# Kernel optimization log

Hardware: AMD Instinct MI355X
Metric: run time of the kernel (lower is better)

Reference implementation:

```python
import jax, jax.numpy as jnp
import numpy as np

N_SRC = 1_000_000
N_OUT = 65_536
D = 64

def setup_inputs() -> dict:
    key = jax.random.key(0)
    k1, k2, k3 = jax.random.split(key, 3)
    input = jax.random.normal(k1, (N_OUT, D), dtype=jnp.float32)
    index = jax.random.randint(k2, (N_SRC, D), 0, N_OUT, dtype=jnp.int64)
    src = jax.random.normal(k3, (N_SRC, D), dtype=jnp.float32)
    return {"input": input, "index": index, "src": src}

def reference(input, index, src):
    # torch.scatter_reduce(input, 0, index, src, reduce='sum', include_self=True):
    #   out = input.copy(); out[index[i, j], j] += src[i, j]
    cols = jnp.arange(src.shape[1])[None, :]  # [1, D] broadcasts against index [N, D]
    return input.at[index, cols].add(src)
```

## Files before the change

kernel.cpp:

```cpp
#include <hip/hip_runtime.h>


typedef unsigned int u32;
typedef unsigned short u16;
typedef unsigned long long u64;

#define NBKT 256
#define NBLK 1024
#define BLK  512
#define BATCH 2048
#define CAPR 320
#define CAPS 30
#define CPAD 31
#define FU   16
#define TILE 16384
#define OMAX 130048

__global__ void Zero_kernel(u32* p, int n) {
    int i = threadIdx.x;
    if (i < n) p[i] = 0;
}

__global__ void InitOut_kernel(const float4* __restrict__ in, float4* __restrict__ out, int n4) {
    int i = blockIdx.x * blockDim.x + threadIdx.x;
    if (i < n4) out[i] = in[i];
}

__global__ void FallbackAdd_kernel(const int4* __restrict__ index4,
                                   const float4* __restrict__ src4,
                                   float* __restrict__ out, int n4) {
    const int stride = gridDim.x * blockDim.x;
    for (int i = blockIdx.x * blockDim.x + threadIdx.x; i < n4; i += stride) {
        int4 idx = index4[i];
        float4 v = src4[i];
        int jbase = (i & 15) << 2;
        atomicAdd(&out[(idx.x << 6) + jbase + 0], v.x);
        atomicAdd(&out[(idx.y << 6) + jbase + 1], v.y);
        atomicAdd(&out[(idx.z << 6) + jbase + 2], v.z);
        atomicAdd(&out[(idx.w << 6) + jbase + 3], v.w);
    }
}

__global__ __launch_bounds__(BLK) void Scatter_kernel(
        const int* __restrict__ index, const float* __restrict__ src,
        float* __restrict__ val, u16* __restrict__ dst, u16* __restrict__ cntg,
        u32* __restrict__ ocnt, u64* __restrict__ olist,
        int epb, long long E)
{
    __shared__ float sv[NBKT][CPAD];
    __shared__ u16  sd[NBKT][CPAD];
    __shared__ u32  cnt[NBKT];
    __shared__ u32  flushed[NBKT];
    const int t = threadIdx.x;
    const int k = blockIdx.x;
    long long c0 = (long long)k * epb;
    long long c1 = c0 + epb; if (c1 > E) c1 = E;
    if (c0 >= c1) {
        if (t < NBKT) cntg[(size_t)k * NBKT + t] = 0;
        return;
    }
    if (t < NBKT) { cnt[t] = 0; flushed[t] = 0; }
    __syncthreads();

    const int col0 = (t << 2) & 63;
    const size_t rbase = (size_t)k * CAPR;

#define PROC(rr, vv, cc) { \
    int bb = (rr) >> 8; \
    u32 p = atomicAdd(&cnt[bb], 1u); \
    if (p < CAPR) { \
        u32 fl = flushed[bb]; \
        u32 slot = p - fl; \
        u16 dd = (u16)((((rr) & 255) << 6) | (cc)); \
        if (slot < CAPS) { sv[bb][slot] = (vv); sd[bb][slot] = dd; } \
        else { size_t pos = (size_t)bb * (NBLK * CAPR) + rbase + p; \
               val[pos] = (vv); dst[pos] = dd; } \
    } else { \
        u32 oi = atomicAdd(ocnt, 1u); \
        if (oi < OMAX) \
            olist[oi] = ((u64)__float_as_uint(vv) << 32) | (u32)(((rr) << 6) + (cc)); \
    } }

    long long e = c0 + t * 4;
    int4 r; float4 v;
    bool have = e < c1;
    if (have) { r = *(const int4*)(index + e); v = *(const float4*)(src + e); }

    const int g = t >> 3, lr = t & 7;

    for (long long eb = c0; eb < c1; eb += BATCH) {
        if (have) {
            PROC(r.x, v.x, col0 + 0);
            PROC(r.y, v.y, col0 + 1);
            PROC(r.z, v.z, col0 + 2);
            PROC(r.w, v.w, col0 + 3);
        }
        long long en = e + BATCH;
        bool haveN = en < c1;
        int4 rn; float4 vn;
        if (haveN) { rn = *(const int4*)(index + en); vn = *(const float4*)(src + en); }
        __syncthreads();
        #pragma unroll
        for (int pass = 0; pass < 4; ++pass) {
            int b = (pass << 6) + g;
            u32 c = cnt[b]; if (c > CAPR) c = CAPR;
            u32 fl = flushed[b];
            u32 staged = c - fl;
            u32 fcopy, rem, newfl;
            if (staged > CAPS) { fcopy = CAPS; rem = 0; newfl = c; }
            else { fcopy = staged & ~(FU - 1u); rem = staged - fcopy; newfl = fl + fcopy; }
            size_t rb = (size_t)b * (NBLK * CAPR) + rbase + fl;
            for (u32 i = lr; i < fcopy; i += 8) {
                val[rb + i] = sv[b][i];
                dst[rb + i] = sd[b][i];
            }
            for (u32 i = lr; i < rem; i += 8) {
                sv[b][i] = sv[b][fcopy + i];
                sd[b][i] = sd[b][fcopy + i];
            }
            if (lr == 0) flushed[b] = newfl;
        }
        __syncthreads();
        r = rn; v = vn; have = haveN; e = en;
    }

    #pragma unroll
    for (int pass = 0; pass < 4; ++pass) {
        int b = (pass << 6) + g;
        u32 c = cnt[b]; if (c > CAPR) c = CAPR;
        u32 fl = flushed[b];
        u32 staged = c - fl;
        u32 fcopy = staged > CAPS ? CAPS : staged;
        size_t rb = (size_t)b * (NBLK * CAPR) + rbase + fl;
        for (u32 i = lr; i < fcopy; i += 8) {
            val[rb + i] = sv[b][i];
            dst[rb + i] = sd[b][i];
        }
    }
    __syncthreads();
    if (t < NBKT) {
        u32 c = cnt[t]; if (c > CAPR) c = CAPR;
        cntg[(size_t)k * NBKT + t] = (u16)c;
    }
#undef PROC
}

__global__ __launch_bounds__(512) void Reduce_kernel(
        const float* __restrict__ val, const u16* __restrict__ dst,
        const u16* __restrict__ cntg, const u32* __restrict__ ocnt,
        const u64* __restrict__ olist, float* __restrict__ out)
{
    __shared__ float tile[TILE];
    const int b = blockIdx.x >> 1;
    const int p = blockIdx.x & 1;
    const int t = threadIdx.x;
    float4* t4 = (float4*)tile;
    for (int i = t; i < TILE / 4; i += 512) t4[i] = make_float4(0.f, 0.f, 0.f, 0.f);
    __syncthreads();
    const int g = t >> 3, lr = t & 7;
    const size_t bb = (size_t)b * ((size_t)NBLK * CAPR);
    for (int k = p * (NBLK / 2) + g; k < (p + 1) * (NBLK / 2); k += 64) {
        u32 n = cntg[(size_t)k * NBKT + b]; if (n > CAPR) n = CAPR;
        const float* vp = val + bb + (size_t)k * CAPR;
        const u16*  dp = dst + bb + (size_t)k * CAPR;
        u32 n4 = n & ~3u;
        for (u32 i = lr * 4; i + 4 <= n4 + 4 && i < n4; i += 32) {
            float4 v = *(const float4*)(vp + i);
            ushort4 d = *(const ushort4*)(dp + i);
            atomicAdd(&tile[d.x], v.x);
            atomicAdd(&tile[d.y], v.y);
            atomicAdd(&tile[d.z], v.z);
            atomicAdd(&tile[d.w], v.w);
        }
        u32 rem = n - n4;
        if ((u32)lr < rem)
            atomicAdd(&tile[dp[n4 + lr]], vp[n4 + lr]);
    }
    if (p == 0) {
        u32 on = *ocnt; if (on > OMAX) on = OMAX;
        for (u32 i = t; i < on; i += 512) {
            u64 pr = olist[i];
            u32 d = (u32)pr;
            if ((d >> 14) == (u32)b)
                atomicAdd(&tile[d & (TILE - 1)], __uint_as_float((u32)(pr >> 32)));
        }
    }
    __syncthreads();
    float* ob = out + (size_t)b * TILE;
    for (int i = t; i < TILE; i += 512)
        atomicAdd(&ob[i], tile[i]);
}

extern "C" void kernel_launch(void* const* d_in, const int* in_sizes, int n_in,
                              void* d_out, int out_size, void* d_ws, size_t ws_size,
                              hipStream_t stream) {
    const float* input = (const float*)d_in[0];
    const int*   index = (const int*)d_in[1];
    const float* src   = (const float*)d_in[2];
    float* out = (float*)d_out;
    long long E = (long long)in_sizes[2];

    const size_t off_olist = 64;
    const size_t off_cnt   = off_olist + (size_t)OMAX * 8;
    const size_t off_val   = (size_t)2u << 20;
    const size_t off_dst   = off_val + (size_t)NBKT * NBLK * CAPR * 4;
    const size_t need      = off_dst + (size_t)NBKT * NBLK * CAPR * 2;

    int epb = (int)(((E + NBLK - 1) / NBLK + 63) & ~63LL);

    int n4o = out_size / 4;
    if (ws_size < need || (E & 3) || out_size != NBKT * TILE || epb > 65536) {
        InitOut_kernel<<<(n4o + 255) / 256, 256, 0, stream>>>(
            (const float4*)input, (float4*)out, n4o);
        FallbackAdd_kernel<<<2048, 256, 0, stream>>>(
            (const int4*)index, (const float4*)src, out, (int)(E / 4));
        return;
    }

    char* ws = (char*)d_ws;
    u32*  ocnt  = (u32*)ws;
    u64*  olist = (u64*)(ws + off_olist);
    u16*  cntg  = (u16*)(ws + off_cnt);
    float* val  = (float*)(ws + off_val);
    u16*  dst   = (u16*)(ws + off_dst);

    Zero_kernel<<<1, 64, 0, stream>>>(ocnt, 16);
    InitOut_kernel<<<(n4o + 255) / 256, 256, 0, stream>>>(
        (const float4*)input, (float4*)out, n4o);

    Scatter_kernel<<<NBLK, BLK, 0, stream>>>(index, src, val, dst, cntg,
                                             ocnt, olist, epb, E);
    Reduce_kernel<<<NBKT * 2, 512, 0, stream>>>(val, dst, cntg, ocnt, olist, out);
}
```

Baseline: 622.6 us.

## Rework scatter staging to flush fixed chunks and widen reduce blocks

The per-bucket shared-memory staging in the scatter kernel now counts entries in the current staging buffer only, with a separate running total of flushed entries. Full buffers are flushed whole and partial buffers flush a fixed 16-entry chunk using float2/u32 vector stores. This is meant to reduce scattered direct global writes and narrow stores. Overflow beyond the per-block capacity is routed to the overflow list at flush time. The reduce kernel moves from 512 to 1024 threads per block to raise parallelism, at the cost of more shared-memory atomic contention per tile.

```diff
diff --git a/kernel.cpp b/kernel.cpp
--- a/kernel.cpp
+++ b/kernel.cpp
@@ -50,7 +50,7 @@
     __shared__ float sv[NBKT][CPAD];
     __shared__ u16  sd[NBKT][CPAD];
     __shared__ u32  cnt[NBKT];
-    __shared__ u32  flushed[NBKT];
+    __shared__ u32  fltot[NBKT];
     const int t = threadIdx.x;
     const int k = blockIdx.x;
     long long c0 = (long long)k * epb;
@@ -59,7 +59,7 @@
         if (t < NBKT) cntg[(size_t)k * NBKT + t] = 0;
         return;
     }
-    if (t < NBKT) { cnt[t] = 0; flushed[t] = 0; }
+    if (t < NBKT) { cnt[t] = 0; fltot[t] = 0; }
     __syncthreads();
 
     const int col0 = (t << 2) & 63;
@@ -68,18 +68,13 @@
 #define PROC(rr, vv, cc) { \
     int bb = (rr) >> 8; \
     u32 p = atomicAdd(&cnt[bb], 1u); \
-    if (p < CAPR) { \
-        u32 fl = flushed[bb]; \
-        u32 slot = p - fl; \
-        u16 dd = (u16)((((rr) & 255) << 6) | (cc)); \
-        if (slot < CAPS) { sv[bb][slot] = (vv); sd[bb][slot] = dd; } \
-        else { size_t pos = (size_t)bb * (NBLK * CAPR) + rbase + p; \
-               val[pos] = (vv); dst[pos] = dd; } \
-    } else { \
-        u32 oi = atomicAdd(ocnt, 1u); \
-        if (oi < OMAX) \
-            olist[oi] = ((u64)__float_as_uint(vv) << 32) | (u32)(((rr) << 6) + (cc)); \
-    } }
+    u16 dd = (u16)((((rr) & 255) << 6) | (cc)); \
+    if (p < CAPS) { sv[bb][p] = (vv); sd[bb][p] = dd; } \
+    else { u32 q = fltot[bb] + p; \
+        if (q < CAPR) { size_t pos = (size_t)bb * (NBLK * CAPR) + rbase + q; \
+                        val[pos] = (vv); dst[pos] = dd; } \
+        else { u32 oi = atomicAdd(ocnt, 1u); \
+               if (oi < OMAX) olist[oi] = ((u64)__float_as_uint(vv) << 32) | (u32)(((rr) << 6) + (cc)); } } }
 
     long long e = c0 + t * 4;
     int4 r; float4 v;
@@ -103,22 +98,47 @@
         #pragma unroll
         for (int pass = 0; pass < 4; ++pass) {
             int b = (pass << 6) + g;
-            u32 c = cnt[b]; if (c > CAPR) c = CAPR;
-            u32 fl = flushed[b];
-            u32 staged = c - fl;
-            u32 fcopy, rem, newfl;
-            if (staged > CAPS) { fcopy = CAPS; rem = 0; newfl = c; }
-            else { fcopy = staged & ~(FU - 1u); rem = staged - fcopy; newfl = fl + fcopy; }
-            size_t rb = (size_t)b * (NBLK * CAPR) + rbase + fl;
-            for (u32 i = lr; i < fcopy; i += 8) {
-                val[rb + i] = sv[b][i];
-                dst[rb + i] = sd[b][i];
+            u32 c = cnt[b];
+            u32 fl = fltot[b];
+            if (c > CAPS) {
+                for (u32 i = lr; i < CAPS; i += 8) {
+                    u32 q = fl + i;
+                    if (q < CAPR) {
+                        size_t pos = (size_t)b * (NBLK * CAPR) + rbase + q;
+                        val[pos] = sv[b][i]; dst[pos] = sd[b][i];
+                    } else {
+                        u32 oi = atomicAdd(ocnt, 1u);
+                        if (oi < OMAX)
+                            olist[oi] = ((u64)__float_as_uint(sv[b][i]) << 32) |
+                                        (u32)(((u32)b << 14) | sd[b][i]);
+                    }
+                }
+                if (lr == 0) { fltot[b] = fl + c; cnt[b] = 0; }
+            } else if (c >= FU) {
+                u32 q = fl + 2 * lr;
+                if (q + 1 < CAPR) {
+                    float2 v2; v2.x = sv[b][2 * lr]; v2.y = sv[b][2 * lr + 1];
+                    u32 d2 = (u32)sd[b][2 * lr] | ((u32)sd[b][2 * lr + 1] << 16);
+                    size_t pos = (size_t)b * (NBLK * CAPR) + rbase + q;
+                    *(float2*)&val[pos] = v2;
+                    *(u32*)&dst[pos] = d2;
+                } else {
+                    for (int jj = 0; jj < 2; ++jj) {
+                        u32 qq = q + jj;
+                        u32 oi = atomicAdd(ocnt, 1u);
+                        if (oi < OMAX)
+                            olist[oi] = ((u64)__float_as_uint(sv[b][2 * lr + jj]) << 32) |
+                                        (u32)(((u32)b << 14) | sd[b][2 * lr + jj]);
+                        (void)qq;
+                    }
+                }
+                u32 rem = c - FU;
+                for (u32 i = lr; i < rem; i += 8) {
+                    sv[b][i] = sv[b][FU + i];
+                    sd[b][i] = sd[b][FU + i];
+                }
+                if (lr == 0) { fltot[b] = fl + FU; cnt[b] = rem; }
             }
-            for (u32 i = lr; i < rem; i += 8) {
-                sv[b][i] = sv[b][fcopy + i];
-                sd[b][i] = sd[b][fcopy + i];
-            }
-            if (lr == 0) flushed[b] = newfl;
         }
         __syncthreads();
         r = rn; v = vn; have = haveN; e = en;
@@ -127,25 +147,31 @@
     #pragma unroll
     for (int pass = 0; pass < 4; ++pass) {
         int b = (pass << 6) + g;
-        u32 c = cnt[b]; if (c > CAPR) c = CAPR;
-        u32 fl = flushed[b];
-        u32 staged = c - fl;
-        u32 fcopy = staged > CAPS ? CAPS : staged;
-        size_t rb = (size_t)b * (NBLK * CAPR) + rbase + fl;
-        for (u32 i = lr; i < fcopy; i += 8) {
-            val[rb + i] = sv[b][i];
-            dst[rb + i] = sd[b][i];
+        u32 c = cnt[b]; if (c > CAPS) c = CAPS;
+        u32 fl = fltot[b];
+        for (u32 i = lr; i < c; i += 8) {
+            u32 q = fl + i;
+            if (q < CAPR) {
+                size_t pos = (size_t)b * (NBLK * CAPR) + rbase + q;
+                val[pos] = sv[b][i]; dst[pos] = sd[b][i];
+            } else {
+                u32 oi = atomicAdd(ocnt, 1u);
+                if (oi < OMAX)
+                    olist[oi] = ((u64)__float_as_uint(sv[b][i]) << 32) |
+                                (u32)(((u32)b << 14) | sd[b][i]);
+            }
         }
     }
     __syncthreads();
     if (t < NBKT) {
-        u32 c = cnt[t]; if (c > CAPR) c = CAPR;
-        cntg[(size_t)k * NBKT + t] = (u16)c;
+        u32 total = fltot[t] + cnt[t];
+        if (total > CAPR) total = CAPR;
+        cntg[(size_t)k * NBKT + t] = (u16)total;
     }
 #undef PROC
 }
 
-__global__ __launch_bounds__(512) void Reduce_kernel(
+__global__ __launch_bounds__(1024) void Reduce_kernel(
         const float* __restrict__ val, const u16* __restrict__ dst,
         const u16* __restrict__ cntg, const u32* __restrict__ ocnt,
         const u64* __restrict__ olist, float* __restrict__ out)
@@ -155,16 +181,16 @@
     const int p = blockIdx.x & 1;
     const int t = threadIdx.x;
     float4* t4 = (float4*)tile;
-    for (int i = t; i < TILE / 4; i += 512) t4[i] = make_float4(0.f, 0.f, 0.f, 0.f);
+    for (int i = t; i < TILE / 4; i += 1024) t4[i] = make_float4(0.f, 0.f, 0.f, 0.f);
     __syncthreads();
     const int g = t >> 3, lr = t & 7;
     const size_t bb = (size_t)b * ((size_t)NBLK * CAPR);
-    for (int k = p * (NBLK / 2) + g; k < (p + 1) * (NBLK / 2); k += 64) {
+    for (int k = p * (NBLK / 2) + g; k < (p + 1) * (NBLK / 2); k += 128) {
         u32 n = cntg[(size_t)k * NBKT + b]; if (n > CAPR) n = CAPR;
         const float* vp = val + bb + (size_t)k * CAPR;
         const u16*  dp = dst + bb + (size_t)k * CAPR;
         u32 n4 = n & ~3u;
-        for (u32 i = lr * 4; i + 4 <= n4 + 4 && i < n4; i += 32) {
+        for (u32 i = lr * 4; i < n4; i += 32) {
             float4 v = *(const float4*)(vp + i);
             ushort4 d = *(const ushort4*)(dp + i);
             atomicAdd(&tile[d.x], v.x);
@@ -178,7 +204,7 @@
     }
     if (p == 0) {
         u32 on = *ocnt; if (on > OMAX) on = OMAX;
-        for (u32 i = t; i < on; i += 512) {
+        for (u32 i = t; i < on; i += 1024) {
             u64 pr = olist[i];
             u32 d = (u32)pr;
             if ((d >> 14) == (u32)b)
@@ -187,7 +213,7 @@
     }
     __syncthreads();
     float* ob = out + (size_t)b * TILE;
-    for (int i = t; i < TILE; i += 512)
+    for (int i = t; i < TILE; i += 1024)
         atomicAdd(&ob[i], tile[i]);
 }
 
@@ -230,5 +256,5 @@
 
     Scatter_kernel<<<NBLK, BLK, 0, stream>>>(index, src, val, dst, cntg,
                                              ocnt, olist, epb, E);
-    Reduce_kernel<<<NBKT * 2, 512, 0, stream>>>(val, dst, cntg, ocnt, olist, out);
-}
+    Reduce_kernel<<<NBKT * 2, 1024, 0, stream>>>(val, dst, cntg, ocnt, olist, out);
+}
```

Result: no change. 625.8 us (+0.5%).
